# Performance work log

Hardware: AMD Instinct MI355X
Metric: run time of the kernel (lower is better)

Reference implementation:

```python
import jax, jax.numpy as jnp
import numpy as np

N = 20000      # nodes
E = 320000     # edges (avg degree 16)
G = 256        # graphs
F_NODE = 64
F_EDGE = 16
HID = 256
H, C = 4, 64   # heads, per-head channels
EPS = 1e-5


def setup_inputs() -> dict:
    key = jax.random.key(0)
    ks = jax.random.split(key, 24)
    def rn(k, shape, scale=0.05):
        return jax.random.normal(k, shape, dtype=jnp.float32) * scale
    src = jax.random.randint(ks[0], (E,), 0, N)
    dst = (src + 1 + jax.random.randint(ks[1], (E,), 0, N - 1)) % N  # no pre-existing self loops
    edge_index = jnp.stack([src, dst]).astype(jnp.int32)
    batch = ((jnp.arange(N) * G) // N).astype(jnp.int32)  # contiguous graph ids, all G graphs non-empty
    return {
        'x': rn(ks[2], (N, F_NODE), 1.0),
        'edge_index': edge_index,
        'batch': batch,
        'edge_attr': rn(ks[3], (E, F_EDGE), 1.0),
        'enc_W': rn(ks[4], (F_NODE, HID)),
        'enc_b': jnp.zeros((HID,), jnp.float32),
        'conv_Wl': rn(ks[5], (3, HID, HID)),
        'conv_bl': rn(ks[6], (3, HID)),
        'conv_Wr': rn(ks[7], (3, HID, HID)),
        'conv_br': rn(ks[8], (3, HID)),
        'conv_We': rn(ks[9], (3, F_EDGE, HID)),
        'conv_att': rn(ks[10], (3, H, C)),
        'conv_bias': rn(ks[11], (3, HID)),
        'bn_gamma': jnp.ones((3, HID), jnp.float32),
        'bn_beta': jnp.zeros((3, HID), jnp.float32),
        'bn_mean': rn(ks[12], (3, HID)),
        'bn_var': jax.random.uniform(ks[13], (3, HID), dtype=jnp.float32) + 0.5,
        'cls_W1': rn(ks[14], (2 * HID, HID)),
        'cls_b1': jnp.zeros((HID,), jnp.float32),
        'cls_g1': jnp.ones((HID,), jnp.float32),
        'cls_bt1': jnp.zeros((HID,), jnp.float32),
        'cls_m1': rn(ks[15], (HID,)),
        'cls_v1': jax.random.uniform(ks[16], (HID,), dtype=jnp.float32) + 0.5,
        'cls_W2': rn(ks[17], (HID, HID // 2)),
        'cls_b2': jnp.zeros((HID // 2,), jnp.float32),
        'cls_g2': jnp.ones((HID // 2,), jnp.float32),
        'cls_bt2': jnp.zeros((HID // 2,), jnp.float32),
        'cls_m2': rn(ks[18], (HID // 2,)),
        'cls_v2': jax.random.uniform(ks[19], (HID // 2,), dtype=jnp.float32) + 0.5,
        'cls_W3': rn(ks[20], (HID // 2, 1)),
        'cls_b3': jnp.zeros((1,), jnp.float32),
    }


def _bn(v, g, b, m, var):
    return (v - m) * jax.lax.rsqrt(var + EPS) * g + b


def _gatv2(h, src, dst, eattr, Wl, bl, Wr, br, We, att, bias, n):
    # GATv2Conv (share_weights=False, concat=True) with edge features.
    xl = (h @ Wl + bl).reshape(n, H, C)          # messages come from lin_l(source)
    xr = (h @ Wr + br).reshape(n, H, C)
    ef = (eattr @ We).reshape(-1, H, C)
    z = jax.nn.leaky_relu(xl[src] + xr[dst] + ef, 0.2)   # [E', H, C]
    alpha = jnp.einsum('ehc,hc->eh', z, att)             # [E', H]
    amax = jax.ops.segment_max(alpha, dst, num_segments=n)
    amax = jnp.where(jnp.isfinite(amax), amax, 0.0)
    ex = jnp.exp(alpha - amax[dst])
    den = jax.ops.segment_sum(ex, dst, num_segments=n)
    a = ex / den[dst]                                    # self loops guarantee den > 0
    out = jax.ops.segment_sum(a[:, :, None] * xl[src], dst, num_segments=n)
    return out.reshape(n, H * C) + bias


def reference(x, edge_index, batch, edge_attr, enc_W, enc_b, conv_Wl, conv_bl, conv_Wr, conv_br, conv_We, conv_att, conv_bias, bn_gamma, bn_beta, bn_mean, bn_var, cls_W1, cls_b1, cls_g1, cls_bt1, cls_m1, cls_v1, cls_W2, cls_b2, cls_g2, cls_bt2, cls_m2, cls_v2, cls_W3, cls_b3):
    n = x.shape[0]
    src, dst = edge_index[0], edge_index[1]
    # add self loops with fill_value='mean' (mean of incoming edge_attr per node)
    deg = jax.ops.segment_sum(jnp.ones(src.shape, x.dtype), dst, num_segments=n)
    loop_attr = jax.ops.segment_sum(edge_attr, dst, num_segments=n) / jnp.maximum(deg, 1.0)[:, None]
    loop = jnp.arange(n, dtype=src.dtype)
    src2 = jnp.concatenate([src, loop])
    dst2 = jnp.concatenate([dst, loop])
    ea2 = jnp.concatenate([edge_attr, loop_attr], axis=0)

    h = jax.nn.relu(x @ enc_W + enc_b)
    for i in range(3):  # fixed layer count
        h_in = h
        hc = _gatv2(h, src2, dst2, ea2, conv_Wl[i], conv_bl[i], conv_Wr[i], conv_br[i], conv_We[i], conv_att[i], conv_bias[i], n)
        h = jax.nn.relu(_bn(hc, bn_gamma[i], bn_beta[i], bn_mean[i], bn_var[i])) + h_in

    cnt = jax.ops.segment_sum(jnp.ones((n,), h.dtype), batch, num_segments=G)
    x_mean = jax.ops.segment_sum(h, batch, num_segments=G) / jnp.maximum(cnt, 1.0)[:, None]
    x_max = jax.ops.segment_max(h, batch, num_segments=G)
    xp = jnp.concatenate([x_mean, x_max], axis=1)

    z = jax.nn.relu(_bn(xp @ cls_W1 + cls_b1, cls_g1, cls_bt1, cls_m1, cls_v1))
    z = jax.nn.relu(_bn(z @ cls_W2 + cls_b2, cls_g2, cls_bt2, cls_m2, cls_v2))
    return (z @ cls_W3 + cls_b3)[:, 0]
```

## Files before the change

kernel.cpp:

```cpp
#include <hip/hip_runtime.h>
#include <hip/hip_bf16.h>

#define N_NODES 20000
#define N_EDGES 320000
#define N_E2    (N_EDGES + N_NODES)
#define N_GRAPHS 256
#define HID 256
#define EPS 1e-5f
#define NSCAN 20
#define CPB 4

typedef unsigned short u16;
typedef __attribute__((ext_vector_type(8))) short short8;
typedef __attribute__((ext_vector_type(4))) float f32x4;

__device__ __forceinline__ float b2f(u16 u) {
    union { unsigned int i; float f; } v; v.i = ((unsigned int)u) << 16; return v.f;
}
__device__ __forceinline__ u16 f2b(float f) {
    __hip_bfloat16 h = __float2bfloat16(f);
    return *reinterpret_cast<u16*>(&h);
}

__global__ void k_init(int* cnt, int* cursor) {
    int i = blockIdx.x * 256 + threadIdx.x;
    if (i < N_NODES) { cnt[i] = 1; cursor[i] = 0; }
}

__global__ void k_count(const int* __restrict__ dst, int* __restrict__ cnt) {
    int e = blockIdx.x * 256 + threadIdx.x;
    if (e < N_EDGES) atomicAdd(&cnt[dst[e]], 1);
}

__global__ void k_scan1(const int* __restrict__ cnt, int* __restrict__ rowp, int* __restrict__ part) {
    __shared__ int ls[256];
    int b = blockIdx.x, tid = threadIdx.x;
    int base = b * 1024 + tid * 4;
    int c[4]; int s = 0;
#pragma unroll
    for (int u = 0; u < 4; u++) { int i = base + u; c[u] = (i < N_NODES) ? cnt[i] : 0; s += c[u]; }
    ls[tid] = s; __syncthreads();
    for (int off = 1; off < 256; off <<= 1) {
        int v = (tid >= off) ? ls[tid - off] : 0;
        __syncthreads();
        ls[tid] += v;
        __syncthreads();
    }
    int excl = ls[tid] - s;
#pragma unroll
    for (int u = 0; u < 4; u++) { int i = base + u; if (i < N_NODES) rowp[i] = excl; excl += c[u]; }
    if (tid == 255) part[b] = ls[255];
}

__global__ void k_scan2(int* part, int* rowp) {
    int s = 0;
    for (int b = 0; b < NSCAN; b++) { int v = part[b]; part[b] = s; s += v; }
    rowp[N_NODES] = s;
}

__global__ void k_scan3(int* __restrict__ rowp, const int* __restrict__ part) {
    int b = blockIdx.x, tid = threadIdx.x;
    int add = part[b];
    int base = b * 1024 + tid * 4;
#pragma unroll
    for (int u = 0; u < 4; u++) { int i = base + u; if (i < N_NODES) rowp[i] += add; }
}

__global__ void k_fill(const int* __restrict__ src, const int* __restrict__ dst,
                       const int* __restrict__ rowp, int* __restrict__ cursor,
                       int* __restrict__ csr_src, int* __restrict__ csr_dst,
                       int* __restrict__ csr_aid) {
    int t = blockIdx.x * 256 + threadIdx.x;
    if (t < N_EDGES) {
        int d = dst[t];
        int pos = atomicAdd(&cursor[d], 1);
        int w = rowp[d] + pos;
        csr_src[w] = src[t];
        csr_dst[w] = d;
        csr_aid[w] = t;
    } else if (t < N_E2) {
        int n = t - N_EDGES;
        int pos = atomicAdd(&cursor[n], 1);
        int w = rowp[n] + pos;
        csr_src[w] = n;
        csr_dst[w] = n;
        csr_aid[w] = N_EDGES + n;
    }
}

__global__ void k_pad(int* csr_src, int* csr_dst) {
    int i = threadIdx.x;
    csr_src[N_E2 + i] = 0;
    csr_dst[N_E2 + i] = 0;
}

__global__ void k_loopattr(const int* __restrict__ rowp, const int* __restrict__ csr_aid,
                           const float* __restrict__ edge_attr, float* __restrict__ lattr) {
    int t = blockIdx.x * 256 + threadIdx.x;
    if (t >= N_NODES * 16) return;
    int n = t >> 4, j = t & 15;
    int st = rowp[n], en = rowp[n + 1];
    float s = 0.f;
    for (int i = st; i < en; i++) {
        int aid = csr_aid[i];
        if (aid < N_EDGES) s += edge_attr[(size_t)aid * 16 + j];
    }
    float deg = (float)(en - st - 1);
    lattr[(size_t)n * 16 + j] = s / fmaxf(deg, 1.0f);
}

__global__ void k_eacsr(const int* __restrict__ csr_aid,
                        const float* __restrict__ edge_attr,
                        const float* __restrict__ lattr,
                        u16* __restrict__ ea_bf) {
    int t = blockIdx.x * 256 + threadIdx.x;
    if (t >= N_E2 * 2) return;
    int e = t >> 1, hf = t & 1;
    int aid = csr_aid[e];
    const float* ap = (aid < N_EDGES) ? edge_attr + (size_t)aid * 16
                                      : lattr + (size_t)(aid - N_EDGES) * 16;
    float4 a = ((const float4*)ap)[hf * 2];
    float4 b = ((const float4*)ap)[hf * 2 + 1];
    u16 v[8] = {f2b(a.x), f2b(a.y), f2b(a.z), f2b(a.w),
                f2b(b.x), f2b(b.y), f2b(b.z), f2b(b.w)};
    *(uint4*)(ea_bf + (size_t)t * 8) = *(uint4*)v;
}

__global__ void k_wef(const float* __restrict__ We, u16* __restrict__ Wef) {
    int t = blockIdx.x * 256 + threadIdx.x;
    if (t >= 3 * 16 * 64) return;
    int layer = t >> 10, r = t & 1023;
    int nt = r >> 6, l = r & 63;
    int kc = l >> 4, ch = nt * 16 + (l & 15);
    u16 v[8];
#pragma unroll
    for (int q = 0; q < 8; q++) {
        float x = 0.f;
        if (kc < 2) x = We[(size_t)layer * 4096 + (size_t)(kc * 8 + q) * 256 + ch];
        v[q] = f2b(x);
    }
    *(uint4*)(Wef + (size_t)t * 8) = *(uint4*)v;
}

__global__ void k_xbf(const float* __restrict__ x, u16* __restrict__ xb) {
    int t = blockIdx.x * 256 + threadIdx.x;
    if (t >= N_NODES * 16) return;
    float4 v = ((const float4*)x)[t];
    u16 o[4] = {f2b(v.x), f2b(v.y), f2b(v.z), f2b(v.w)};
    *(ushort4*)(xb + (size_t)t * 4) = *(ushort4*)o;
}

__global__ void k_twg(const float* __restrict__ W, u16* __restrict__ Wt, int K, int N,
                      unsigned int lstride) {
    __shared__ float tile[32][33];
    int layer = blockIdx.z;
    const float* Wp = W + (size_t)layer * K * N;
    u16* Wtp = Wt + (size_t)layer * lstride;
    int bk = blockIdx.x * 32, bn = blockIdx.y * 32;
    int tx = threadIdx.x & 31, ty = threadIdx.x >> 5;
#pragma unroll
    for (int q = 0; q < 4; q++) {
        int k = bk + ty + q * 8;
        tile[ty + q * 8][tx] = Wp[(size_t)k * N + bn + tx];
    }
    __syncthreads();
#pragma unroll
    for (int q = 0; q < 4; q++) {
        int n = bn + ty + q * 8;
        Wtp[(size_t)n * K + bk + tx] = f2b(tile[tx][ty + q * 8]);
    }
}

__global__ void k_blr(const float* __restrict__ bl, const float* __restrict__ br,
                      float* __restrict__ blr) {
    int t = blockIdx.x * 256 + threadIdx.x;
    if (t >= 3 * 512) return;
    int l = t >> 9, c = t & 511;
    blr[t] = (c < 256) ? bl[l * 256 + c] : br[l * 256 + (c - 256)];
}

template <int EPI>
__global__ __launch_bounds__(256) void k_gemm_bf(
    const u16* __restrict__ A, int lda,
    const u16* __restrict__ Bt, int ldb, int K,
    const float* __restrict__ bias,
    u16* __restrict__ Cbf, int ldc, int coff,
    float* __restrict__ Cf, int M)
{
    __shared__ __align__(16) u16 As[128 * 40];
    __shared__ __align__(16) u16 Bs[64 * 40];
    int tid = threadIdx.x;
    int lane = tid & 63, w = tid >> 6;
    int m0 = blockIdx.x * 128, n0 = blockIdx.y * 64;

    f32x4 acc[2][4];
#pragma unroll
    for (int i = 0; i < 2; i++)
#pragma unroll
        for (int j = 0; j < 4; j++) acc[i][j] = (f32x4){0.f, 0.f, 0.f, 0.f};

    int srow = tid >> 2, skc = (tid & 3) * 8;
    int lr = lane & 15, lk = (lane >> 4) * 8;

    int ktiles = K >> 5;
    for (int kt = 0; kt < ktiles; kt++) {
        if (kt) __syncthreads();
#pragma unroll
        for (int q = 0; q < 2; q++) {
            int arow = q * 64 + srow;
            uint4 av = make_uint4(0, 0, 0, 0);
            if (m0 + arow < M)
                av = *(const uint4*)(A + (size_t)(m0 + arow) * lda + kt * 32 + skc);
            *(uint4*)&As[arow * 40 + skc] = av;
        }
        {
            uint4 bv = *(const uint4*)(Bt + (size_t)(n0 + srow) * ldb + kt * 32 + skc);
            *(uint4*)&Bs[srow * 40 + skc] = bv;
        }
        __syncthreads();

        short8 af0 = *(const short8*)&As[(w * 32 + lr) * 40 + lk];
        short8 af1 = *(const short8*)&As[(w * 32 + 16 + lr) * 40 + lk];
        short8 bf[4];
#pragma unroll
        for (int nt = 0; nt < 4; nt++)
            bf[nt] = *(const short8*)&Bs[(nt * 16 + lr) * 40 + lk];
#pragma unroll
        for (int nt = 0; nt < 4; nt++) {
            acc[0][nt] = __builtin_amdgcn_mfma_f32_16x16x32_bf16(af0, bf[nt], acc[0][nt], 0, 0, 0);
            acc[1][nt] = __builtin_amdgcn_mfma_f32_16x16x32_bf16(af1, bf[nt], acc[1][nt], 0, 0, 0);
        }
    }

    int rq = (lane >> 4) * 4;
#pragma unroll
    for (int nt = 0; nt < 4; nt++) {
        int col = n0 + nt * 16 + lr;
        float bv = bias[col];
#pragma unroll
        for (int mt = 0; mt < 2; mt++) {
#pragma unroll
            for (int j = 0; j < 4; j++) {
                int row = m0 + w * 32 + mt * 16 + rq + j;
                if (row < M) {
                    float v = acc[mt][nt][j] + bv;
                    if (EPI == 1) {
                        v = fmaxf(v, 0.f);
                        Cf[(size_t)row * ldc + col] = v;
                        Cbf[(size_t)row * ldc + col] = f2b(v);
                    } else {
                        Cbf[(size_t)row * ldc + coff + col] = f2b(v);
                    }
                }
            }
        }
    }
}

__global__ __launch_bounds__(256) void k_alpha3(
    const u16* __restrict__ xlr,
    const u16* __restrict__ ea_bf,
    const int* __restrict__ csr_src, const int* __restrict__ csr_dst,
    const u16* __restrict__ Wef,
    const float* __restrict__ att,
    float* __restrict__ alpha)
{
    __shared__ __align__(16) u16 wef_s[16 * 64 * 8];
    __shared__ float att_s[256];
    int tid = threadIdx.x, lane = tid & 63, w = tid >> 6;
    {
        const uint4* s = (const uint4*)Wef;
        uint4* d = (uint4*)wef_s;
#pragma unroll
        for (int q = 0; q < 4; q++) d[q * 256 + tid] = s[q * 256 + tid];
        att_s[tid] = att[tid];
    }
    int eg = lane >> 4, t16 = lane & 15;
    __syncthreads();

    for (int it = 0; it < CPB; it++) {
        int chunk = blockIdx.x * CPB + it;
        if (chunk * 64 >= N_E2) break;
        int e_base = chunk * 64 + w * 16;
        int e_raw = e_base + t16;
        int e = (e_raw < N_E2) ? e_raw : N_E2 - 1;

        short8 eafrag = {0, 0, 0, 0, 0, 0, 0, 0};
        if (eg < 2) eafrag = *(const short8*)(ea_bf + (size_t)e * 16 + eg * 8);
        int s = csr_src[e], d = csr_dst[e];
        const u16* xlp = xlr + (size_t)s * 512 + eg * 4;
        const u16* xrp = xlr + (size_t)d * 512 + 256 + eg * 4;

        uint2 xlv[16], xrv[16];
#pragma unroll
        for (int nt = 0; nt < 16; nt++) {
            xlv[nt] = *(const uint2*)(xlp + nt * 16);
            xrv[nt] = *(const uint2*)(xrp + nt * 16);
        }

        float pj = 0.f;
#pragma unroll
        for (int nt = 0; nt < 16; nt++) {
            short8 wfrag = *(const short8*)&wef_s[(nt * 64 + lane) * 8];
            f32x4 D = __builtin_amdgcn_mfma_f32_16x16x32_bf16(
                wfrag, eafrag, (f32x4){0.f, 0.f, 0.f, 0.f}, 0, 0, 0);
            int ch0 = nt * 16 + eg * 4;
            float4 at4 = *(const float4*)&att_s[ch0];
            const u16* xl4 = (const u16*)&xlv[nt];
            const u16* xr4 = (const u16*)&xrv[nt];
#pragma unroll
            for (int j = 0; j < 4; j++) {
                float z = D[j] + b2f(xl4[j]) + b2f(xr4[j]);
                z = fmaxf(z, 0.f) + 0.2f * fminf(z, 0.f);
                pj = fmaf(z, ((const float*)&at4)[j], pj);
            }
            if ((nt & 3) == 3) {
                float p = pj;
                p += __shfl_xor(p, 16, 64);
                p += __shfl_xor(p, 32, 64);
                if (eg == 0 && e_raw < N_E2) alpha[(size_t)e_raw * 4 + (nt >> 2)] = p;
                pj = 0.f;
            }
        }
    }
}

__global__ __launch_bounds__(256) void k_aggr(
    const u16* __restrict__ xlr, const float* __restrict__ alpha,
    const int* __restrict__ rowp, const int* __restrict__ csr_src,
    const float* __restrict__ cbias,
    const float* __restrict__ bng, const float* __restrict__ bnb,
    const float* __restrict__ bnm, const float* __restrict__ bnv,
    float* __restrict__ h, u16* __restrict__ h_bf)
{
    __shared__ float lex[4][64][4];
    __shared__ int   lsrc[4][64];
    int lane = threadIdx.x & 63;
    int wv = threadIdx.x >> 6;
    int n = blockIdx.x * 4 + wv;
    if (n >= N_NODES) return;
    int st = rowp[n], en = rowp[n + 1];
    int hsel = lane >> 4;
    int c0 = lane * 4;

    float m4[4]  = {-3.0e38f, -3.0e38f, -3.0e38f, -3.0e38f};
    float den4[4] = {0.f, 0.f, 0.f, 0.f};
    float acc[4]  = {0.f, 0.f, 0.f, 0.f};

    for (int cs = st; cs < en; cs += 64) {
        int cnt = min(64, en - cs);
        float a4[4];
        int s_i = 0;
        if (lane < cnt) {
            float4 v = *(const float4*)(alpha + (size_t)(cs + lane) * 4);
            a4[0] = v.x; a4[1] = v.y; a4[2] = v.z; a4[3] = v.w;
            s_i = csr_src[cs + lane];
        } else {
            a4[0] = a4[1] = a4[2] = a4[3] = -3.0e38f;
        }
        float cm[4] = {a4[0], a4[1], a4[2], a4[3]};
#pragma unroll
        for (int o = 32; o >= 1; o >>= 1)
#pragma unroll
            for (int u = 0; u < 4; u++) cm[u] = fmaxf(cm[u], __shfl_xor(cm[u], o, 64));
        float sc[4];
#pragma unroll
        for (int u = 0; u < 4; u++) {
            float nm = fmaxf(m4[u], cm[u]);
            sc[u] = __expf(m4[u] - nm);
            den4[u] *= sc[u];
            m4[u] = nm;
        }
        float scl = sc[hsel];
#pragma unroll
        for (int u = 0; u < 4; u++) acc[u] *= scl;
        float ex[4];
#pragma unroll
        for (int u = 0; u < 4; u++) ex[u] = (lane < cnt) ? __expf(a4[u] - m4[u]) : 0.f;
        float sx[4] = {ex[0], ex[1], ex[2], ex[3]};
#pragma unroll
        for (int o = 32; o >= 1; o >>= 1)
#pragma unroll
            for (int u = 0; u < 4; u++) sx[u] += __shfl_xor(sx[u], o, 64);
#pragma unroll
        for (int u = 0; u < 4; u++) den4[u] += sx[u];
        *(float4*)&lex[wv][lane][0] = make_float4(ex[0], ex[1], ex[2], ex[3]);
        lsrc[wv][lane] = s_i;
        int j = 0;
        for (; j + 8 <= cnt; j += 8) {
            float a[8]; int sj[8];
#pragma unroll
            for (int q = 0; q < 8; q++) { a[q] = lex[wv][j + q][hsel]; sj[q] = lsrc[wv][j + q]; }
            ushort4 xg[8];
#pragma unroll
            for (int q = 0; q < 8; q++) xg[q] = *(const ushort4*)(xlr + (size_t)sj[q] * 512 + c0);
#pragma unroll
            for (int q = 0; q < 8; q++) {
                acc[0] += a[q] * b2f(((const u16*)&xg[q])[0]);
                acc[1] += a[q] * b2f(((const u16*)&xg[q])[1]);
                acc[2] += a[q] * b2f(((const u16*)&xg[q])[2]);
                acc[3] += a[q] * b2f(((const u16*)&xg[q])[3]);
            }
        }
        for (; j < cnt; j++) {
            float a = lex[wv][j][hsel];
            int sj = lsrc[wv][j];
            ushort4 xg = *(const ushort4*)(xlr + (size_t)sj * 512 + c0);
            acc[0] += a * b2f(((const u16*)&xg)[0]);
            acc[1] += a * b2f(((const u16*)&xg)[1]);
            acc[2] += a * b2f(((const u16*)&xg)[2]);
            acc[3] += a * b2f(((const u16*)&xg)[3]);
        }
    }

    float dd = den4[hsel];
    float4 hin = *(const float4*)(h + (size_t)n * 256 + c0);
    float4 cb  = *(const float4*)(cbias + c0);
    float4 gg  = *(const float4*)(bng + c0);
    float4 bb  = *(const float4*)(bnb + c0);
    float4 mm  = *(const float4*)(bnm + c0);
    float4 vv  = *(const float4*)(bnv + c0);
    float hi[4] = {hin.x, hin.y, hin.z, hin.w};
    float cbv[4] = {cb.x, cb.y, cb.z, cb.w};
    float gv[4] = {gg.x, gg.y, gg.z, gg.w};
    float bv[4] = {bb.x, bb.y, bb.z, bb.w};
    float mv[4] = {mm.x, mm.y, mm.z, mm.w};
    float vvv[4] = {vv.x, vv.y, vv.z, vv.w};
    float4 o;
    ushort4 ob;
#pragma unroll
    for (int u = 0; u < 4; u++) {
        float val = acc[u] / dd + cbv[u];
        val = (val - mv[u]) * rsqrtf(vvv[u] + EPS) * gv[u] + bv[u];
        val = fmaxf(val, 0.f) + hi[u];
        ((float*)&o)[u] = val;
        ((u16*)&ob)[u] = f2b(val);
    }
    *(float4*)(h + (size_t)n * 256 + c0) = o;
    *(ushort4*)(h_bf + (size_t)n * 256 + c0) = ob;
}

__global__ __launch_bounds__(256) void k_poolp(
    const float* __restrict__ h, float* __restrict__ psum, float* __restrict__ pmax)
{
    int g = blockIdx.x, p = blockIdx.y, c = threadIdx.x;
    int gst = (g * N_NODES + N_GRAPHS - 1) / N_GRAPHS;
    int gen = ((g + 1) * N_NODES + N_GRAPHS - 1) / N_GRAPHS;
    int len = gen - gst;
    int cst = gst + (len * p) / 8;
    int cen = gst + (len * (p + 1)) / 8;
    float s = 0.f, mx = -3.0e38f;
    for (int i = cst; i < cen; i++) {
        float v = h[(size_t)i * 256 + c];
        s += v;
        mx = fmaxf(mx, v);
    }
    psum[(size_t)(g * 8 + p) * 256 + c] = s;
    pmax[(size_t)(g * 8 + p) * 256 + c] = mx;
}

__global__ __launch_bounds__(256) void k_head(
    const float* __restrict__ psum, const float* __restrict__ pmax,
    const float* __restrict__ W1, const float* __restrict__ b1,
    const float* __restrict__ g1, const float* __restrict__ bt1,
    const float* __restrict__ m1, const float* __restrict__ v1,
    const float* __restrict__ W2, const float* __restrict__ b2,
    const float* __restrict__ g2, const float* __restrict__ bt2,
    const float* __restrict__ m2, const float* __restrict__ v2,
    const float* __restrict__ W3, const float* __restrict__ b3,
    float* __restrict__ out)
{
    __shared__ float xp_s[512];
    __shared__ float z1_s[256];
    __shared__ float z2p[2][128];
    __shared__ float z2_s[128];
    int g = blockIdx.x, c = threadIdx.x;
    int gst = (g * N_NODES + N_GRAPHS - 1) / N_GRAPHS;
    int gen = ((g + 1) * N_NODES + N_GRAPHS - 1) / N_GRAPHS;

    float s = 0.f, mx = -3.0e38f;
#pragma unroll
    for (int p = 0; p < 8; p++) {
        s += psum[(size_t)(g * 8 + p) * 256 + c];
        mx = fmaxf(mx, pmax[(size_t)(g * 8 + p) * 256 + c]);
    }
    xp_s[c] = s / (float)(gen - gst);
    xp_s[256 + c] = mx;
    __syncthreads();

    float a0 = 0.f, a1 = 0.f, a2 = 0.f, a3 = 0.f;
#pragma unroll 4
    for (int k = 0; k < 512; k += 4) {
        a0 = fmaf(xp_s[k + 0], W1[(k + 0) * 256 + c], a0);
        a1 = fmaf(xp_s[k + 1], W1[(k + 1) * 256 + c], a1);
        a2 = fmaf(xp_s[k + 2], W1[(k + 2) * 256 + c], a2);
        a3 = fmaf(xp_s[k + 3], W1[(k + 3) * 256 + c], a3);
    }
    float a = (a0 + a1) + (a2 + a3) + b1[c];
    a = (a - m1[c]) * rsqrtf(v1[c] + EPS) * g1[c] + bt1[c];
    z1_s[c] = fmaxf(a, 0.f);
    __syncthreads();

    {
        int c2 = c & 127, half = c >> 7;
        float b_acc = 0.f;
#pragma unroll 4
        for (int k = 0; k < 128; k++) {
            int kk = half * 128 + k;
            b_acc = fmaf(z1_s[kk], W2[kk * 128 + c2], b_acc);
        }
        z2p[half][c2] = b_acc;
    }
    __syncthreads();
    if (c < 128) {
        float a2v = z2p[0][c] + z2p[1][c] + b2[c];
        a2v = (a2v - m2[c]) * rsqrtf(v2[c] + EPS) * g2[c] + bt2[c];
        z2_s[c] = fmaxf(a2v, 0.f);
    }
    __syncthreads();

    if (c < 64) {
        float a3v = z2_s[c] * W3[c] + z2_s[c + 64] * W3[c + 64];
#pragma unroll
        for (int o = 32; o >= 1; o >>= 1) a3v += __shfl_xor(a3v, o, 64);
        if (c == 0) out[g] = a3v + b3[0];
    }
}

extern "C" void kernel_launch(void* const* d_in, const int* in_sizes, int n_in,
                              void* d_out, int out_size, void* d_ws, size_t ws_size,
                              hipStream_t stream) {
    const float* x         = (const float*)d_in[0];
    const int*   ei        = (const int*)d_in[1];
    const int*   src       = ei;
    const int*   dst       = ei + N_EDGES;
    const float* edge_attr = (const float*)d_in[3];
    const float* enc_W     = (const float*)d_in[4];
    const float* enc_b     = (const float*)d_in[5];
    const float* conv_Wl   = (const float*)d_in[6];
    const float* conv_bl   = (const float*)d_in[7];
    const float* conv_Wr   = (const float*)d_in[8];
    const float* conv_br   = (const float*)d_in[9];
    const float* conv_We   = (const float*)d_in[10];
    const float* conv_att  = (const float*)d_in[11];
    const float* conv_bias = (const float*)d_in[12];
    const float* bn_g      = (const float*)d_in[13];
    const float* bn_b      = (const float*)d_in[14];
    const float* bn_m      = (const float*)d_in[15];
    const float* bn_v      = (const float*)d_in[16];
    const float* cls_W1    = (const float*)d_in[17];
    const float* cls_b1    = (const float*)d_in[18];
    const float* cls_g1    = (const float*)d_in[19];
    const float* cls_bt1   = (const float*)d_in[20];
    const float* cls_m1    = (const float*)d_in[21];
    const float* cls_v1    = (const float*)d_in[22];
    const float* cls_W2    = (const float*)d_in[23];
    const float* cls_b2    = (const float*)d_in[24];
    const float* cls_g2    = (const float*)d_in[25];
    const float* cls_bt2   = (const float*)d_in[26];
    const float* cls_m2    = (const float*)d_in[27];
    const float* cls_v2    = (const float*)d_in[28];
    const float* cls_W3    = (const float*)d_in[29];
    const float* cls_b3    = (const float*)d_in[30];
    float* out = (float*)d_out;

    char* ws = (char*)d_ws;
    size_t off = 0;
    auto alloc = [&](size_t bytes) -> void* {
        void* p = ws + off;
        off += (bytes + 255) & ~(size_t)255;
        return p;
    };
    float* h       = (float*)alloc((size_t)N_NODES * 256 * 4);
    u16*   h_bf    = (u16*)alloc((size_t)N_NODES * 256 * 2);
    u16*   xlr_bf  = (u16*)alloc((size_t)N_NODES * 512 * 2);
    float* lattr   = (float*)alloc((size_t)N_NODES * 16 * 4);
    u16*   ea_bf   = (u16*)alloc((size_t)N_E2 * 16 * 2);
    float* alphas  = (float*)alloc((size_t)N_E2 * 4 * 4);
    u16*   x_bf    = (u16*)alloc((size_t)N_NODES * 64 * 2);
    u16*   enc_Wt  = (u16*)alloc((size_t)64 * 256 * 2);
    u16*   Wtlr    = (u16*)alloc((size_t)3 * 512 * 256 * 2);
    float* blr     = (float*)alloc((size_t)3 * 512 * 4);
    u16*   Wef     = (u16*)alloc((size_t)3 * 16 * 64 * 8 * 2);
    float* psum    = (float*)alloc((size_t)N_GRAPHS * 8 * 256 * 4);
    float* pmax    = (float*)alloc((size_t)N_GRAPHS * 8 * 256 * 4);
    int*   cnt     = (int*)alloc((size_t)N_NODES * 4);
    int*   rowp    = (int*)alloc((size_t)(N_NODES + 1) * 4);
    int*   cursor  = (int*)alloc((size_t)N_NODES * 4);
    int*   csr_src = (int*)alloc((size_t)(N_E2 + 512) * 4);
    int*   csr_dst = (int*)alloc((size_t)(N_E2 + 512) * 4);
    int*   csr_aid = (int*)alloc((size_t)N_E2 * 4);
    int*   part    = (int*)alloc(64 * 4);

    k_init<<<(N_NODES + 255) / 256, 256, 0, stream>>>(cnt, cursor);
    k_count<<<(N_EDGES + 255) / 256, 256, 0, stream>>>(dst, cnt);
    k_scan1<<<NSCAN, 256, 0, stream>>>(cnt, rowp, part);
    k_scan2<<<1, 1, 0, stream>>>(part, rowp);
    k_scan3<<<NSCAN, 256, 0, stream>>>(rowp, part);
    k_fill<<<(N_E2 + 255) / 256, 256, 0, stream>>>(src, dst, rowp, cursor, csr_src, csr_dst, csr_aid);
    k_pad<<<1, 512, 0, stream>>>(csr_src, csr_dst);
    k_loopattr<<<(N_NODES * 16 + 255) / 256, 256, 0, stream>>>(rowp, csr_aid, edge_attr, lattr);
    k_eacsr<<<(N_E2 * 2 + 255) / 256, 256, 0, stream>>>(csr_aid, edge_attr, lattr, ea_bf);

    k_xbf<<<(N_NODES * 16 + 255) / 256, 256, 0, stream>>>(x, x_bf);
    k_twg<<<dim3(2, 8, 1), 256, 0, stream>>>(enc_W, enc_Wt, 64, 256, 64 * 256);
    k_twg<<<dim3(8, 8, 3), 256, 0, stream>>>(conv_Wl, Wtlr, 256, 256, 512 * 256);
    k_twg<<<dim3(8, 8, 3), 256, 0, stream>>>(conv_Wr, Wtlr + 256 * 256, 256, 256, 512 * 256);
    k_blr<<<6, 256, 0, stream>>>(conv_bl, conv_br, blr);
    k_wef<<<12, 256, 0, stream>>>(conv_We, Wef);

    dim3 ggrid((N_NODES + 127) / 128, 4);
    dim3 ggrid2((N_NODES + 127) / 128, 8);
    k_gemm_bf<1><<<ggrid, 256, 0, stream>>>(x_bf, 64, enc_Wt, 64, 64,
                                            enc_b, h_bf, 256, 0, h, N_NODES);

    int nchunks = (N_E2 + 63) / 64;
    int ablocks = (nchunks + CPB - 1) / CPB;
    for (int i = 0; i < 3; i++) {
        k_gemm_bf<0><<<ggrid2, 256, 0, stream>>>(h_bf, 256, Wtlr + (size_t)i * 131072, 256, 256,
                                                 blr + (size_t)i * 512, xlr_bf, 512, 0, nullptr, N_NODES);
        k_alpha3<<<ablocks, 256, 0, stream>>>(
            xlr_bf, ea_bf, csr_src, csr_dst,
            Wef + (size_t)i * 8192, conv_att + (size_t)i * 256, alphas);
        k_aggr<<<N_NODES / 4, 256, 0, stream>>>(
            xlr_bf, alphas, rowp, csr_src,
            conv_bias + (size_t)i * HID,
            bn_g + (size_t)i * HID, bn_b + (size_t)i * HID,
            bn_m + (size_t)i * HID, bn_v + (size_t)i * HID, h, h_bf);
    }

    k_poolp<<<dim3(N_GRAPHS, 8), 256, 0, stream>>>(h, psum, pmax);
    k_head<<<N_GRAPHS, 256, 0, stream>>>(
        psum, pmax, cls_W1, cls_b1, cls_g1, cls_bt1, cls_m1, cls_v1,
        cls_W2, cls_b2, cls_g2, cls_bt2, cls_m2, cls_v2,
        cls_W3, cls_b3, out);
}
```

Baseline: 481.7 us.

## Fuse GATv2 attention scoring and softmax aggregation into one per-node kernel

Merges the per-edge attention-logit kernel and the per-node aggregation kernel into a single kernel where each wavefront handles one destination node and walks its CSR edges in chunks of 16. The source-node features gathered for scoring are reused for the weighted aggregation, and the destination features are staged once in shared memory. This removes the alpha buffer round-trip, the csr_dst array, the padding kernel and one launch per layer. In exchange it uses online softmax with many cross-lane shuffles per edge chunk, and load balance now follows node degree. Each block also reloads the edge-weight tile into shared memory for only four nodes.

```diff
diff --git a/kernel.cpp b/kernel.cpp
--- a/kernel.cpp
+++ b/kernel.cpp
@@ -8,7 +8,6 @@
 #define HID 256
 #define EPS 1e-5f
 #define NSCAN 20
-#define CPB 4
 
 typedef unsigned short u16;
 typedef __attribute__((ext_vector_type(8))) short short8;
@@ -68,30 +67,21 @@
 
 __global__ void k_fill(const int* __restrict__ src, const int* __restrict__ dst,
                        const int* __restrict__ rowp, int* __restrict__ cursor,
-                       int* __restrict__ csr_src, int* __restrict__ csr_dst,
-                       int* __restrict__ csr_aid) {
+                       int* __restrict__ csr_src, int* __restrict__ csr_aid) {
     int t = blockIdx.x * 256 + threadIdx.x;
     if (t < N_EDGES) {
         int d = dst[t];
         int pos = atomicAdd(&cursor[d], 1);
         int w = rowp[d] + pos;
         csr_src[w] = src[t];
-        csr_dst[w] = d;
         csr_aid[w] = t;
     } else if (t < N_E2) {
         int n = t - N_EDGES;
         int pos = atomicAdd(&cursor[n], 1);
         int w = rowp[n] + pos;
         csr_src[w] = n;
-        csr_dst[w] = n;
         csr_aid[w] = N_EDGES + n;
     }
-}
-
-__global__ void k_pad(int* csr_src, int* csr_dst) {
-    int i = threadIdx.x;
-    csr_src[N_E2 + i] = 0;
-    csr_dst[N_E2 + i] = 0;
 }
 
 __global__ void k_loopattr(const int* __restrict__ rowp, const int* __restrict__ csr_aid,
@@ -257,47 +247,53 @@
     }
 }
 
-__global__ __launch_bounds__(256) void k_alpha3(
+__global__ __launch_bounds__(256) void k_gat(
     const u16* __restrict__ xlr,
     const u16* __restrict__ ea_bf,
-    const int* __restrict__ csr_src, const int* __restrict__ csr_dst,
+    const int* __restrict__ csr_src, const int* __restrict__ rowp,
     const u16* __restrict__ Wef,
     const float* __restrict__ att,
-    float* __restrict__ alpha)
+    const float* __restrict__ cbias,
+    const float* __restrict__ bng, const float* __restrict__ bnb,
+    const float* __restrict__ bnm, const float* __restrict__ bnv,
+    float* __restrict__ h, u16* __restrict__ h_bf)
 {
     __shared__ __align__(16) u16 wef_s[16 * 64 * 8];
     __shared__ float att_s[256];
-    int tid = threadIdx.x, lane = tid & 63, w = tid >> 6;
+    __shared__ __align__(16) u16 xr_s[4][256];
+    int tid = threadIdx.x, lane = tid & 63, wv = tid >> 6;
+    int eg = lane >> 4, t16 = lane & 15;
+    int n = blockIdx.x * 4 + wv;
+
     {
         const uint4* s = (const uint4*)Wef;
-        uint4* d = (uint4*)wef_s;
-#pragma unroll
-        for (int q = 0; q < 4; q++) d[q * 256 + tid] = s[q * 256 + tid];
+        uint4* dptr = (uint4*)wef_s;
+#pragma unroll
+        for (int q = 0; q < 4; q++) dptr[q * 256 + tid] = s[q * 256 + tid];
         att_s[tid] = att[tid];
     }
-    int eg = lane >> 4, t16 = lane & 15;
+    *(uint2*)&xr_s[wv][lane * 4] = *(const uint2*)(xlr + (size_t)n * 512 + 256 + lane * 4);
     __syncthreads();
 
-    for (int it = 0; it < CPB; it++) {
-        int chunk = blockIdx.x * CPB + it;
-        if (chunk * 64 >= N_E2) break;
-        int e_base = chunk * 64 + w * 16;
-        int e_raw = e_base + t16;
-        int e = (e_raw < N_E2) ? e_raw : N_E2 - 1;
+    int st = rowp[n], en = rowp[n + 1];
+    float m4[4]  = {-3.0e38f, -3.0e38f, -3.0e38f, -3.0e38f};
+    float den4[4] = {0.f, 0.f, 0.f, 0.f};
+    float acc[4]  = {0.f, 0.f, 0.f, 0.f};
+
+    for (int cs = st; cs < en; cs += 16) {
+        int cnt = en - cs; if (cnt > 16) cnt = 16;
+        int e = cs + ((t16 < cnt) ? t16 : (cnt - 1));
 
         short8 eafrag = {0, 0, 0, 0, 0, 0, 0, 0};
         if (eg < 2) eafrag = *(const short8*)(ea_bf + (size_t)e * 16 + eg * 8);
-        int s = csr_src[e], d = csr_dst[e];
+        int s = csr_src[e];
         const u16* xlp = xlr + (size_t)s * 512 + eg * 4;
-        const u16* xrp = xlr + (size_t)d * 512 + 256 + eg * 4;
-
-        uint2 xlv[16], xrv[16];
-#pragma unroll
-        for (int nt = 0; nt < 16; nt++) {
-            xlv[nt] = *(const uint2*)(xlp + nt * 16);
-            xrv[nt] = *(const uint2*)(xrp + nt * 16);
-        }
-
+
+        uint2 xlv[16];
+#pragma unroll
+        for (int nt = 0; nt < 16; nt++) xlv[nt] = *(const uint2*)(xlp + nt * 16);
+
+        float al[4];
         float pj = 0.f;
 #pragma unroll
         for (int nt = 0; nt < 16; nt++) {
@@ -306,8 +302,9 @@
                 wfrag, eafrag, (f32x4){0.f, 0.f, 0.f, 0.f}, 0, 0, 0);
             int ch0 = nt * 16 + eg * 4;
             float4 at4 = *(const float4*)&att_s[ch0];
+            uint2 xr2 = *(const uint2*)&xr_s[wv][ch0];
             const u16* xl4 = (const u16*)&xlv[nt];
-            const u16* xr4 = (const u16*)&xrv[nt];
+            const u16* xr4 = (const u16*)&xr2;
 #pragma unroll
             for (int j = 0; j < 4; j++) {
                 float z = D[j] + b2f(xl4[j]) + b2f(xr4[j]);
@@ -318,121 +315,69 @@
                 float p = pj;
                 p += __shfl_xor(p, 16, 64);
                 p += __shfl_xor(p, 32, 64);
-                if (eg == 0 && e_raw < N_E2) alpha[(size_t)e_raw * 4 + (nt >> 2)] = p;
+                al[nt >> 2] = p;
                 pj = 0.f;
             }
         }
-    }
-}
-
-__global__ __launch_bounds__(256) void k_aggr(
-    const u16* __restrict__ xlr, const float* __restrict__ alpha,
-    const int* __restrict__ rowp, const int* __restrict__ csr_src,
-    const float* __restrict__ cbias,
-    const float* __restrict__ bng, const float* __restrict__ bnb,
-    const float* __restrict__ bnm, const float* __restrict__ bnv,
-    float* __restrict__ h, u16* __restrict__ h_bf)
-{
-    __shared__ float lex[4][64][4];
-    __shared__ int   lsrc[4][64];
-    int lane = threadIdx.x & 63;
-    int wv = threadIdx.x >> 6;
-    int n = blockIdx.x * 4 + wv;
-    if (n >= N_NODES) return;
-    int st = rowp[n], en = rowp[n + 1];
-    int hsel = lane >> 4;
-    int c0 = lane * 4;
-
-    float m4[4]  = {-3.0e38f, -3.0e38f, -3.0e38f, -3.0e38f};
-    float den4[4] = {0.f, 0.f, 0.f, 0.f};
-    float acc[4]  = {0.f, 0.f, 0.f, 0.f};
-
-    for (int cs = st; cs < en; cs += 64) {
-        int cnt = min(64, en - cs);
-        float a4[4];
-        int s_i = 0;
-        if (lane < cnt) {
-            float4 v = *(const float4*)(alpha + (size_t)(cs + lane) * 4);
-            a4[0] = v.x; a4[1] = v.y; a4[2] = v.z; a4[3] = v.w;
-            s_i = csr_src[cs + lane];
-        } else {
-            a4[0] = a4[1] = a4[2] = a4[3] = -3.0e38f;
-        }
-        float cm[4] = {a4[0], a4[1], a4[2], a4[3]};
-#pragma unroll
-        for (int o = 32; o >= 1; o >>= 1)
-#pragma unroll
-            for (int u = 0; u < 4; u++) cm[u] = fmaxf(cm[u], __shfl_xor(cm[u], o, 64));
-        float sc[4];
+        if (t16 >= cnt) { al[0] = al[1] = al[2] = al[3] = -3.0e38f; }
+
+        float sc[4], ex[4];
 #pragma unroll
         for (int u = 0; u < 4; u++) {
-            float nm = fmaxf(m4[u], cm[u]);
+            float cm = al[u];
+            cm = fmaxf(cm, __shfl_xor(cm, 1, 64));
+            cm = fmaxf(cm, __shfl_xor(cm, 2, 64));
+            cm = fmaxf(cm, __shfl_xor(cm, 4, 64));
+            cm = fmaxf(cm, __shfl_xor(cm, 8, 64));
+            float nm = fmaxf(m4[u], cm);
             sc[u] = __expf(m4[u] - nm);
-            den4[u] *= sc[u];
+            ex[u] = (t16 < cnt) ? __expf(al[u] - nm) : 0.f;
+            float sx = ex[u];
+            sx += __shfl_xor(sx, 1, 64);
+            sx += __shfl_xor(sx, 2, 64);
+            sx += __shfl_xor(sx, 4, 64);
+            sx += __shfl_xor(sx, 8, 64);
+            den4[u] = den4[u] * sc[u] + sx;
             m4[u] = nm;
         }
-        float scl = sc[hsel];
-#pragma unroll
-        for (int u = 0; u < 4; u++) acc[u] *= scl;
-        float ex[4];
-#pragma unroll
-        for (int u = 0; u < 4; u++) ex[u] = (lane < cnt) ? __expf(a4[u] - m4[u]) : 0.f;
-        float sx[4] = {ex[0], ex[1], ex[2], ex[3]};
-#pragma unroll
-        for (int o = 32; o >= 1; o >>= 1)
-#pragma unroll
-            for (int u = 0; u < 4; u++) sx[u] += __shfl_xor(sx[u], o, 64);
-#pragma unroll
-        for (int u = 0; u < 4; u++) den4[u] += sx[u];
-        *(float4*)&lex[wv][lane][0] = make_float4(ex[0], ex[1], ex[2], ex[3]);
-        lsrc[wv][lane] = s_i;
-        int j = 0;
-        for (; j + 8 <= cnt; j += 8) {
-            float a[8]; int sj[8];
-#pragma unroll
-            for (int q = 0; q < 8; q++) { a[q] = lex[wv][j + q][hsel]; sj[q] = lsrc[wv][j + q]; }
-            ushort4 xg[8];
-#pragma unroll
-            for (int q = 0; q < 8; q++) xg[q] = *(const ushort4*)(xlr + (size_t)sj[q] * 512 + c0);
-#pragma unroll
-            for (int q = 0; q < 8; q++) {
-                acc[0] += a[q] * b2f(((const u16*)&xg[q])[0]);
-                acc[1] += a[q] * b2f(((const u16*)&xg[q])[1]);
-                acc[2] += a[q] * b2f(((const u16*)&xg[q])[2]);
-                acc[3] += a[q] * b2f(((const u16*)&xg[q])[3]);
+        float scl = sc[t16 >> 2];
+        acc[0] *= scl; acc[1] *= scl; acc[2] *= scl; acc[3] *= scl;
+
+#pragma unroll
+        for (int nt = 0; nt < 16; nt++) {
+            float w = ex[nt >> 2];
+            const u16* xl4 = (const u16*)&xlv[nt];
+            float v0 = w * b2f(xl4[0]);
+            float v1 = w * b2f(xl4[1]);
+            float v2 = w * b2f(xl4[2]);
+            float v3 = w * b2f(xl4[3]);
+#pragma unroll
+            for (int o = 1; o <= 8; o <<= 1) {
+                v0 += __shfl_xor(v0, o, 64);
+                v1 += __shfl_xor(v1, o, 64);
+                v2 += __shfl_xor(v2, o, 64);
+                v3 += __shfl_xor(v3, o, 64);
             }
-        }
-        for (; j < cnt; j++) {
-            float a = lex[wv][j][hsel];
-            int sj = lsrc[wv][j];
-            ushort4 xg = *(const ushort4*)(xlr + (size_t)sj * 512 + c0);
-            acc[0] += a * b2f(((const u16*)&xg)[0]);
-            acc[1] += a * b2f(((const u16*)&xg)[1]);
-            acc[2] += a * b2f(((const u16*)&xg)[2]);
-            acc[3] += a * b2f(((const u16*)&xg)[3]);
-        }
-    }
-
-    float dd = den4[hsel];
+            if (t16 == nt) { acc[0] += v0; acc[1] += v1; acc[2] += v2; acc[3] += v3; }
+        }
+    }
+
+    int c0 = t16 * 16 + eg * 4;
+    float dd = den4[t16 >> 2];
     float4 hin = *(const float4*)(h + (size_t)n * 256 + c0);
     float4 cb  = *(const float4*)(cbias + c0);
     float4 gg  = *(const float4*)(bng + c0);
     float4 bb  = *(const float4*)(bnb + c0);
     float4 mm  = *(const float4*)(bnm + c0);
     float4 vv  = *(const float4*)(bnv + c0);
-    float hi[4] = {hin.x, hin.y, hin.z, hin.w};
-    float cbv[4] = {cb.x, cb.y, cb.z, cb.w};
-    float gv[4] = {gg.x, gg.y, gg.z, gg.w};
-    float bv[4] = {bb.x, bb.y, bb.z, bb.w};
-    float mv[4] = {mm.x, mm.y, mm.z, mm.w};
-    float vvv[4] = {vv.x, vv.y, vv.z, vv.w};
     float4 o;
     ushort4 ob;
 #pragma unroll
     for (int u = 0; u < 4; u++) {
-        float val = acc[u] / dd + cbv[u];
-        val = (val - mv[u]) * rsqrtf(vvv[u] + EPS) * gv[u] + bv[u];
-        val = fmaxf(val, 0.f) + hi[u];
+        float val = acc[u] / dd + ((const float*)&cb)[u];
+        val = (val - ((const float*)&mm)[u]) * rsqrtf(((const float*)&vv)[u] + EPS)
+              * ((const float*)&gg)[u] + ((const float*)&bb)[u];
+        val = fmaxf(val, 0.f) + ((const float*)&hin)[u];
         ((float*)&o)[u] = val;
         ((u16*)&ob)[u] = f2b(val);
     }
@@ -576,7 +521,6 @@
     u16*   xlr_bf  = (u16*)alloc((size_t)N_NODES * 512 * 2);
     float* lattr   = (float*)alloc((size_t)N_NODES * 16 * 4);
     u16*   ea_bf   = (u16*)alloc((size_t)N_E2 * 16 * 2);
-    float* alphas  = (float*)alloc((size_t)N_E2 * 4 * 4);
     u16*   x_bf    = (u16*)alloc((size_t)N_NODES * 64 * 2);
     u16*   enc_Wt  = (u16*)alloc((size_t)64 * 256 * 2);
     u16*   Wtlr    = (u16*)alloc((size_t)3 * 512 * 256 * 2);
@@ -587,8 +531,7 @@
     int*   cnt     = (int*)alloc((size_t)N_NODES * 4);
     int*   rowp    = (int*)alloc((size_t)(N_NODES + 1) * 4);
     int*   cursor  = (int*)alloc((size_t)N_NODES * 4);
-    int*   csr_src = (int*)alloc((size_t)(N_E2 + 512) * 4);
-    int*   csr_dst = (int*)alloc((size_t)(N_E2 + 512) * 4);
+    int*   csr_src = (int*)alloc((size_t)N_E2 * 4);
     int*   csr_aid = (int*)alloc((size_t)N_E2 * 4);
     int*   part    = (int*)alloc(64 * 4);
 
@@ -597,8 +540,7 @@
     k_scan1<<<NSCAN, 256, 0, stream>>>(cnt, rowp, part);
     k_scan2<<<1, 1, 0, stream>>>(part, rowp);
     k_scan3<<<NSCAN, 256, 0, stream>>>(rowp, part);
-    k_fill<<<(N_E2 + 255) / 256, 256, 0, stream>>>(src, dst, rowp, cursor, csr_src, csr_dst, csr_aid);
-    k_pad<<<1, 512, 0, stream>>>(csr_src, csr_dst);
+    k_fill<<<(N_E2 + 255) / 256, 256, 0, stream>>>(src, dst, rowp, cursor, csr_src, csr_aid);
     k_loopattr<<<(N_NODES * 16 + 255) / 256, 256, 0, stream>>>(rowp, csr_aid, edge_attr, lattr);
     k_eacsr<<<(N_E2 * 2 + 255) / 256, 256, 0, stream>>>(csr_aid, edge_attr, lattr, ea_bf);
 
@@ -614,16 +556,12 @@
     k_gemm_bf<1><<<ggrid, 256, 0, stream>>>(x_bf, 64, enc_Wt, 64, 64,
                                             enc_b, h_bf, 256, 0, h, N_NODES);
 
-    int nchunks = (N_E2 + 63) / 64;
-    int ablocks = (nchunks + CPB - 1) / CPB;
     for (int i = 0; i < 3; i++) {
         k_gemm_bf<0><<<ggrid2, 256, 0, stream>>>(h_bf, 256, Wtlr + (size_t)i * 131072, 256, 256,
                                                  blr + (size_t)i * 512, xlr_bf, 512, 0, nullptr, N_NODES);
-        k_alpha3<<<ablocks, 256, 0, stream>>>(
-            xlr_bf, ea_bf, csr_src, csr_dst,
-            Wef + (size_t)i * 8192, conv_att + (size_t)i * 256, alphas);
-        k_aggr<<<N_NODES / 4, 256, 0, stream>>>(
-            xlr_bf, alphas, rowp, csr_src,
+        k_gat<<<N_NODES / 4, 256, 0, stream>>>(
+            xlr_bf, ea_bf, csr_src, rowp,
+            Wef + (size_t)i * 8192, conv_att + (size_t)i * 256,
             conv_bias + (size_t)i * HID,
             bn_g + (size_t)i * HID, bn_b + (size_t)i * HID,
             bn_m + (size_t)i * HID, bn_v + (size_t)i * HID, h, h_bf);
```

After: 1.162 ms. 2.41x slower.

## Transpose MFMA operands in alpha kernel so each lane owns four edges

Applied to the files above, without the earlier changes.

Swaps the MFMA A/B operands in the attention-logit kernel so each lane holds one channel for four edges rather than four channels for one edge. Edge source and destination indices are now fetched as int4 vector loads, and the attention vector moves from shared memory into registers. The aim is to cut index-load and LDS traffic. In exchange, the feature gathers become scalar 2-byte loads, there are four times as many of them, and each head's reduction needs more shuffles. The int4 index loads in the final partial chunk can also read past the end of the index arrays.

```diff
diff --git a/kernel.cpp b/kernel.cpp
--- a/kernel.cpp
+++ b/kernel.cpp
@@ -266,60 +266,64 @@
     float* __restrict__ alpha)
 {
     __shared__ __align__(16) u16 wef_s[16 * 64 * 8];
-    __shared__ float att_s[256];
     int tid = threadIdx.x, lane = tid & 63, w = tid >> 6;
     {
         const uint4* s = (const uint4*)Wef;
         uint4* d = (uint4*)wef_s;
 #pragma unroll
         for (int q = 0; q < 4; q++) d[q * 256 + tid] = s[q * 256 + tid];
-        att_s[tid] = att[tid];
     }
     int eg = lane >> 4, t16 = lane & 15;
+
+    float att_r[16];
+#pragma unroll
+    for (int q = 0; q < 16; q++) att_r[q] = att[q * 16 + t16];
     __syncthreads();
 
     for (int it = 0; it < CPB; it++) {
         int chunk = blockIdx.x * CPB + it;
         if (chunk * 64 >= N_E2) break;
         int e_base = chunk * 64 + w * 16;
-        int e_raw = e_base + t16;
-        int e = (e_raw < N_E2) ? e_raw : N_E2 - 1;
-
-        short8 eafrag = {0, 0, 0, 0, 0, 0, 0, 0};
-        if (eg < 2) eafrag = *(const short8*)(ea_bf + (size_t)e * 16 + eg * 8);
-        int s = csr_src[e], d = csr_dst[e];
-        const u16* xlp = xlr + (size_t)s * 512 + eg * 4;
-        const u16* xrp = xlr + (size_t)d * 512 + 256 + eg * 4;
-
-        uint2 xlv[16], xrv[16];
+
+        short8 afrag = {0, 0, 0, 0, 0, 0, 0, 0};
+        if (eg < 2) {
+            int e = e_base + t16; if (e > N_E2 - 1) e = N_E2 - 1;
+            afrag = *(const short8*)(ea_bf + (size_t)e * 16 + eg * 8);
+        }
+        int4 s4 = *(const int4*)(csr_src + e_base + eg * 4);
+        int4 d4 = *(const int4*)(csr_dst + e_base + eg * 4);
+        const u16* xlp[4]; const u16* xrp[4];
+        xlp[0] = xlr + (size_t)s4.x * 512;       xlp[1] = xlr + (size_t)s4.y * 512;
+        xlp[2] = xlr + (size_t)s4.z * 512;       xlp[3] = xlr + (size_t)s4.w * 512;
+        xrp[0] = xlr + (size_t)d4.x * 512 + 256; xrp[1] = xlr + (size_t)d4.y * 512 + 256;
+        xrp[2] = xlr + (size_t)d4.z * 512 + 256; xrp[3] = xlr + (size_t)d4.w * 512 + 256;
+
+        float pj[4] = {0.f, 0.f, 0.f, 0.f};
 #pragma unroll
         for (int nt = 0; nt < 16; nt++) {
-            xlv[nt] = *(const uint2*)(xlp + nt * 16);
-            xrv[nt] = *(const uint2*)(xrp + nt * 16);
-        }
-
-        float pj = 0.f;
-#pragma unroll
-        for (int nt = 0; nt < 16; nt++) {
-            short8 wfrag = *(const short8*)&wef_s[(nt * 64 + lane) * 8];
+            short8 bfrag = *(const short8*)&wef_s[(nt * 64 + lane) * 8];
             f32x4 D = __builtin_amdgcn_mfma_f32_16x16x32_bf16(
-                wfrag, eafrag, (f32x4){0.f, 0.f, 0.f, 0.f}, 0, 0, 0);
-            int ch0 = nt * 16 + eg * 4;
-            float4 at4 = *(const float4*)&att_s[ch0];
-            const u16* xl4 = (const u16*)&xlv[nt];
-            const u16* xr4 = (const u16*)&xrv[nt];
+                afrag, bfrag, (f32x4){0.f, 0.f, 0.f, 0.f}, 0, 0, 0);
+            int ch = nt * 16 + t16;
 #pragma unroll
             for (int j = 0; j < 4; j++) {
-                float z = D[j] + b2f(xl4[j]) + b2f(xr4[j]);
+                float z = D[j] + b2f(xlp[j][ch]) + b2f(xrp[j][ch]);
                 z = fmaxf(z, 0.f) + 0.2f * fminf(z, 0.f);
-                pj = fmaf(z, ((const float*)&at4)[j], pj);
+                pj[j] = fmaf(z, att_r[nt], pj[j]);
             }
             if ((nt & 3) == 3) {
-                float p = pj;
-                p += __shfl_xor(p, 16, 64);
-                p += __shfl_xor(p, 32, 64);
-                if (eg == 0 && e_raw < N_E2) alpha[(size_t)e_raw * 4 + (nt >> 2)] = p;
-                pj = 0.f;
+                int hh = nt >> 2;
+#pragma unroll
+                for (int j = 0; j < 4; j++) {
+                    float p = pj[j];
+                    p += __shfl_xor(p, 1, 64);
+                    p += __shfl_xor(p, 2, 64);
+                    p += __shfl_xor(p, 4, 64);
+                    p += __shfl_xor(p, 8, 64);
+                    int e = e_base + eg * 4 + j;
+                    if (t16 == 0 && e < N_E2) alpha[(size_t)e * 4 + hh] = p;
+                    pj[j] = 0.f;
+                }
             }
         }
     }
```

Measured after the change: 452.4 us. -6.1%, faster.
